# Kernel optimization log

Measured on AMD Instinct MI355X. Metric: run time of the kernel, lower is better.

## Reference

```python
import jax, jax.numpy as jnp
import numpy as np

N = 100000      # num_nodes
E = 1600000     # num_edges (avg degree 16)
IN = 128        # in_channels
HID = 8         # hidden_channels (per head)
HEADS = 8
OUT = 64        # out_channels
NEG_SLOPE = 0.2


def setup_inputs() -> dict:
    key = jax.random.key(0)
    ks = jax.random.split(key, 11)
    s = 0.05
    return {
        "x": jax.random.normal(ks[0], (N, IN), jnp.float32),
        "edge_index": jax.random.randint(ks[1], (2, E), 0, N, dtype=jnp.int32),
        "W1": jax.random.normal(ks[2], (IN, HEADS * HID), jnp.float32) * s,
        "a_src1": jax.random.normal(ks[3], (HEADS, HID), jnp.float32) * s,
        "a_dst1": jax.random.normal(ks[4], (HEADS, HID), jnp.float32) * s,
        "b1": jnp.zeros((HEADS * HID,), jnp.float32),
        "W2": jax.random.normal(ks[5], (HEADS * HID, OUT), jnp.float32) * s,
        "a_src2": jax.random.normal(ks[6], (1, OUT), jnp.float32) * s,
        "a_dst2": jax.random.normal(ks[7], (1, OUT), jnp.float32) * s,
        "b2": jnp.zeros((OUT,), jnp.float32),
    }


def gat_conv(x, src, dst, W, a_src, a_dst, bias, heads, out_ch):
    """PyG GATConv (concat=True, dropout=0, self-loops already in src/dst)."""
    n = x.shape[0]
    h = (x @ W).reshape(n, heads, out_ch)               # [N, H, C]
    al_src = jnp.einsum('nhc,hc->nh', h, a_src)          # [N, H]
    al_dst = jnp.einsum('nhc,hc->nh', h, a_dst)          # [N, H]
    e = jax.nn.leaky_relu(al_src[src] + al_dst[dst], NEG_SLOPE)  # [E, H]
    # segment softmax over destination nodes (numerically stable)
    e_max = jax.ops.segment_max(e, dst, num_segments=n)  # [N, H]
    ex = jnp.exp(e - e_max[dst])
    denom = jax.ops.segment_sum(ex, dst, num_segments=n)
    alpha = ex / (denom[dst] + 1e-16)                    # [E, H]
    msg = h[src] * alpha[:, :, None]                     # [E, H, C]
    out = jax.ops.segment_sum(msg, dst, num_segments=n)  # [N, H, C]
    return out.reshape(n, heads * out_ch) + bias


def reference(x, edge_index, W1, a_src1, a_dst1, b1, W2, a_src2, a_dst2, b2):
    n = x.shape[0]
    loops = jnp.arange(n, dtype=edge_index.dtype)
    src = jnp.concatenate([edge_index[0], loops])        # add self-loops (PyG default)
    dst = jnp.concatenate([edge_index[1], loops])
    h = gat_conv(x, src, dst, W1, a_src1, a_dst1, b1, HEADS, HID)
    h = jax.nn.elu(h)
    out = gat_conv(h, src, dst, W2, a_src2, a_dst2, b2, 1, OUT)
    return out
```

## Files before the change

### kernel.cpp

```cpp
#include <hip/hip_runtime.h>
#include <hip/hip_bf16.h>

#define IN_CH   128
#define HEADS   8
#define HID     8
#define MID_CH  64
#define OUT_CH  64
#define CAP     64
#define NRANGE  8

typedef unsigned short u16;
__device__ __forceinline__ u16 f2bu(float f) {
    union { float f; unsigned int i; } v; v.f = f;
    unsigned int lsb = (v.i >> 16) & 1u;
    return (u16)((v.i + 0x7fffu + lsb) >> 16);
}
__device__ __forceinline__ float2 up2(unsigned int u) {
    union { unsigned int i; float f; } a, b;
    a.i = u << 16; b.i = u & 0xffff0000u;
    return make_float2(a.f, b.f);
}
__device__ __forceinline__ float lrelu(float e) { return (e > 0.f) ? e : 0.2f * e; }

__global__ void k0_init(int* __restrict__ deg, int N) {
    int n = blockIdx.x * blockDim.x + threadIdx.x;
    if (n < N) deg[n] = 0;
}

__global__ __launch_bounds__(256) void k1_fill(
    const int* __restrict__ src, const int* __restrict__ dst,
    int* __restrict__ deg, int* __restrict__ adj, int E, int N) {
    int range = blockIdx.x & (NRANGE - 1);
    int chunk = blockIdx.x >> 3;
    int lo = (int)(((long long)N * range) >> 3);
    int hi = (int)(((long long)N * (range + 1)) >> 3);
    int t = chunk * 256 + threadIdx.x;
    int base = t * 4;
    if (base + 3 < E) {
        int4 d4 = *(const int4*)(dst + base);
        int4 s4 = *(const int4*)(src + base);
        if (d4.x >= lo && d4.x < hi) { int p = atomicAdd(&deg[d4.x], 1); if (p < CAP) adj[d4.x * CAP + p] = s4.x; }
        if (d4.y >= lo && d4.y < hi) { int p = atomicAdd(&deg[d4.y], 1); if (p < CAP) adj[d4.y * CAP + p] = s4.y; }
        if (d4.z >= lo && d4.z < hi) { int p = atomicAdd(&deg[d4.z], 1); if (p < CAP) adj[d4.z * CAP + p] = s4.z; }
        if (d4.w >= lo && d4.w < hi) { int p = atomicAdd(&deg[d4.w], 1); if (p < CAP) adj[d4.w * CAP + p] = s4.w; }
    } else {
        for (int j = 0; j < 4; j++) {
            int e = base + j;
            if (e < E) {
                int d = dst[e];
                if (d >= lo && d < hi) {
                    int p = atomicAdd(&deg[d], 1);
                    if (p < CAP) adj[d * CAP + p] = src[e];
                }
            }
        }
    }
}

__global__ __launch_bounds__(256) void k2_gemm1(
    const float* __restrict__ x, const float* __restrict__ W1,
    const float* __restrict__ a_src, const float* __restrict__ a_dst,
    u16* __restrict__ h1b, float* __restrict__ als, float* __restrict__ ald, int N)
{
    __shared__ float Wl[IN_CH * MID_CH];
    __shared__ float xl[16 * IN_CH];
    int tid = threadIdx.x;
    {
        const float4* W4 = (const float4*)W1;
        float4* Wl4 = (float4*)Wl;
        for (int i = tid; i < IN_CH * MID_CH / 4; i += 256) Wl4[i] = W4[i];
    }
    int base = blockIdx.x * 16;
    {
        float4* xl4 = (float4*)xl;
        const float4* x4 = (const float4*)x;
        for (int i = tid; i < 16 * IN_CH / 4; i += 256) {
            int r = i >> 5;
            int n = base + r;
            xl4[i] = (n < N) ? x4[(size_t)n * (IN_CH / 4) + (i & 31)]
                             : make_float4(0.f, 0.f, 0.f, 0.f);
        }
    }
    __syncthreads();

    int wave = tid >> 6, lane = tid & 63;
    int r0 = wave * 4;
    float acc[4] = {0.f, 0.f, 0.f, 0.f};
    const float* x0 = &xl[(r0 + 0) * IN_CH];
    const float* x1 = &xl[(r0 + 1) * IN_CH];
    const float* x2 = &xl[(r0 + 2) * IN_CH];
    const float* x3 = &xl[(r0 + 3) * IN_CH];
    #pragma unroll 8
    for (int k = 0; k < IN_CH; k++) {
        float w = Wl[k * MID_CH + lane];
        acc[0] += x0[k] * w;
        acc[1] += x1[k] * w;
        acc[2] += x2[k] * w;
        acc[3] += x3[k] * w;
    }
    float asv = a_src[lane];
    float adv = a_dst[lane];
    #pragma unroll
    for (int g = 0; g < 4; g++) {
        int n = base + r0 + g;
        if (n >= N) continue;
        h1b[(size_t)n * MID_CH + lane] = f2bu(acc[g]);
        float vs = acc[g] * asv;
        float vd = acc[g] * adv;
        vs += __shfl_xor(vs, 1); vs += __shfl_xor(vs, 2); vs += __shfl_xor(vs, 4);
        vd += __shfl_xor(vd, 1); vd += __shfl_xor(vd, 2); vd += __shfl_xor(vd, 4);
        if ((lane & 7) == 0) {
            als[n * HEADS + (lane >> 3)] = vs;
            ald[n * HEADS + (lane >> 3)] = vd;
        }
    }
}

__global__ __launch_bounds__(256) void k3_agg1(
    const int* __restrict__ deg, const int* __restrict__ adj,
    const u16* __restrict__ h1b, const float* __restrict__ als,
    const float* __restrict__ ald, const float* __restrict__ b1,
    float* __restrict__ h2, int N)
{
    __shared__ int adjl[4][CAP];
    int wave = threadIdx.x >> 6, lane = threadIdx.x & 63;
    int n = blockIdx.x * 4 + wave;
    bool valid = (n < N);
    int nc = valid ? n : (N - 1);

    int g = lane >> 3;
    int c8 = lane & 7;
    int dg = deg[nc]; if (dg > CAP) dg = CAP;
    if (lane < dg) adjl[wave][lane] = adj[(size_t)nc * CAP + lane];
    float aldv = ald[nc * HEADS + c8];
    __syncthreads();

    const uint4* h1v = (const uint4*)h1b;
    float acc[8] = {0,0,0,0,0,0,0,0};
    float denom = 0.f;
    for (int i = g; i < dg; i += 8) {
        int s = adjl[wave][i];
        float ex = __expf(lrelu(als[s * HEADS + c8] + aldv));
        uint4 q = h1v[(size_t)s * 8 + c8];
        float2 p0 = up2(q.x), p1 = up2(q.y), p2 = up2(q.z), p3 = up2(q.w);
        denom += ex;
        acc[0] += ex * p0.x; acc[1] += ex * p0.y;
        acc[2] += ex * p1.x; acc[3] += ex * p1.y;
        acc[4] += ex * p2.x; acc[5] += ex * p2.y;
        acc[6] += ex * p3.x; acc[7] += ex * p3.y;
    }
    if (g == 0) {
        float ex = __expf(lrelu(als[nc * HEADS + c8] + aldv));
        uint4 q = h1v[(size_t)nc * 8 + c8];
        float2 p0 = up2(q.x), p1 = up2(q.y), p2 = up2(q.z), p3 = up2(q.w);
        denom += ex;
        acc[0] += ex * p0.x; acc[1] += ex * p0.y;
        acc[2] += ex * p1.x; acc[3] += ex * p1.y;
        acc[4] += ex * p2.x; acc[5] += ex * p2.y;
        acc[6] += ex * p3.x; acc[7] += ex * p3.y;
    }
    denom += __shfl_xor(denom, 8); denom += __shfl_xor(denom, 16); denom += __shfl_xor(denom, 32);
    #pragma unroll
    for (int j = 0; j < 8; j++) {
        acc[j] += __shfl_xor(acc[j], 8);
        acc[j] += __shfl_xor(acc[j], 16);
        acc[j] += __shfl_xor(acc[j], 32);
    }
    float inv = 1.f / (denom + 1e-16f);

    if (g == 0 && valid) {
        const float4* b4 = (const float4*)b1;
        float4 bl = b4[c8 * 2], bh = b4[c8 * 2 + 1];
        float4 o0, o1;
        o0.x = acc[0] * inv + bl.x; o0.y = acc[1] * inv + bl.y;
        o0.z = acc[2] * inv + bl.z; o0.w = acc[3] * inv + bl.w;
        o1.x = acc[4] * inv + bh.x; o1.y = acc[5] * inv + bh.y;
        o1.z = acc[6] * inv + bh.z; o1.w = acc[7] * inv + bh.w;
        o0.x = (o0.x > 0.f) ? o0.x : (__expf(o0.x) - 1.f);
        o0.y = (o0.y > 0.f) ? o0.y : (__expf(o0.y) - 1.f);
        o0.z = (o0.z > 0.f) ? o0.z : (__expf(o0.z) - 1.f);
        o0.w = (o0.w > 0.f) ? o0.w : (__expf(o0.w) - 1.f);
        o1.x = (o1.x > 0.f) ? o1.x : (__expf(o1.x) - 1.f);
        o1.y = (o1.y > 0.f) ? o1.y : (__expf(o1.y) - 1.f);
        o1.z = (o1.z > 0.f) ? o1.z : (__expf(o1.z) - 1.f);
        o1.w = (o1.w > 0.f) ? o1.w : (__expf(o1.w) - 1.f);
        float4* h2v = (float4*)h2;
        h2v[(size_t)n * 16 + c8 * 2]     = o0;
        h2v[(size_t)n * 16 + c8 * 2 + 1] = o1;
    }
}

__global__ __launch_bounds__(256) void k4_gemm2(
    const float* __restrict__ h2, const float* __restrict__ W2,
    const float* __restrict__ a_src, const float* __restrict__ a_dst,
    u16* __restrict__ t2b, float* __restrict__ als, float* __restrict__ ald, int N)
{
    __shared__ float Wl[MID_CH * OUT_CH];
    __shared__ float xl[16 * MID_CH];
    int tid = threadIdx.x;
    {
        const float4* W4 = (const float4*)W2;
        float4* Wl4 = (float4*)Wl;
        for (int i = tid; i < MID_CH * OUT_CH / 4; i += 256) Wl4[i] = W4[i];
    }
    int base = blockIdx.x * 16;
    {
        float4* xl4 = (float4*)xl;
        const float4* x4 = (const float4*)h2;
        for (int i = tid; i < 16 * MID_CH / 4; i += 256) {
            int r = i >> 4;
            int n = base + r;
            xl4[i] = (n < N) ? x4[(size_t)n * (MID_CH / 4) + (i & 15)]
                             : make_float4(0.f, 0.f, 0.f, 0.f);
        }
    }
    __syncthreads();

    int wave = tid >> 6, lane = tid & 63;
    int r0 = wave * 4;
    float acc[4] = {0.f, 0.f, 0.f, 0.f};
    const float* x0 = &xl[(r0 + 0) * MID_CH];
    const float* x1 = &xl[(r0 + 1) * MID_CH];
    const float* x2 = &xl[(r0 + 2) * MID_CH];
    const float* x3 = &xl[(r0 + 3) * MID_CH];
    #pragma unroll 8
    for (int k = 0; k < MID_CH; k++) {
        float w = Wl[k * OUT_CH + lane];
        acc[0] += x0[k] * w;
        acc[1] += x1[k] * w;
        acc[2] += x2[k] * w;
        acc[3] += x3[k] * w;
    }
    float asv = a_src[lane];
    float adv = a_dst[lane];
    #pragma unroll
    for (int g = 0; g < 4; g++) {
        int n = base + r0 + g;
        if (n >= N) continue;
        t2b[(size_t)n * OUT_CH + lane] = f2bu(acc[g]);
        float vs = acc[g] * asv;
        float vd = acc[g] * adv;
        #pragma unroll
        for (int off = 1; off < 64; off <<= 1) {
            vs += __shfl_xor(vs, off);
            vd += __shfl_xor(vd, off);
        }
        if (lane == 0) { als[n] = vs; ald[n] = vd; }
    }
}

__global__ __launch_bounds__(256) void k5_agg2(
    const int* __restrict__ deg, const int* __restrict__ adj,
    const u16* __restrict__ t2b, const float* __restrict__ als,
    const float* __restrict__ ald, const float* __restrict__ b2,
    float* __restrict__ out, int N)
{
    __shared__ int adjl[4][CAP];
    int wave = threadIdx.x >> 6, lane = threadIdx.x & 63;
    int n = blockIdx.x * 4 + wave;
    bool valid = (n < N);
    int nc = valid ? n : (N - 1);

    int g = lane >> 3;
    int c8 = lane & 7;
    int dg = deg[nc]; if (dg > CAP) dg = CAP;
    if (lane < dg) adjl[wave][lane] = adj[(size_t)nc * CAP + lane];
    float aldv = ald[nc];
    __syncthreads();

    const uint4* t2v = (const uint4*)t2b;
    float acc[8] = {0,0,0,0,0,0,0,0};
    float denom = 0.f;
    for (int i = g; i < dg; i += 8) {
        int s = adjl[wave][i];
        float ex = __expf(lrelu(als[s] + aldv));
        uint4 q = t2v[(size_t)s * 8 + c8];
        float2 p0 = up2(q.x), p1 = up2(q.y), p2 = up2(q.z), p3 = up2(q.w);
        denom += ex;
        acc[0] += ex * p0.x; acc[1] += ex * p0.y;
        acc[2] += ex * p1.x; acc[3] += ex * p1.y;
        acc[4] += ex * p2.x; acc[5] += ex * p2.y;
        acc[6] += ex * p3.x; acc[7] += ex * p3.y;
    }
    if (g == 0) {
        float ex = __expf(lrelu(als[nc] + aldv));
        uint4 q = t2v[(size_t)nc * 8 + c8];
        float2 p0 = up2(q.x), p1 = up2(q.y), p2 = up2(q.z), p3 = up2(q.w);
        denom += ex;
        acc[0] += ex * p0.x; acc[1] += ex * p0.y;
        acc[2] += ex * p1.x; acc[3] += ex * p1.y;
        acc[4] += ex * p2.x; acc[5] += ex * p2.y;
        acc[6] += ex * p3.x; acc[7] += ex * p3.y;
    }
    denom += __shfl_xor(denom, 8); denom += __shfl_xor(denom, 16); denom += __shfl_xor(denom, 32);
    #pragma unroll
    for (int j = 0; j < 8; j++) {
        acc[j] += __shfl_xor(acc[j], 8);
        acc[j] += __shfl_xor(acc[j], 16);
        acc[j] += __shfl_xor(acc[j], 32);
    }
    float inv = 1.f / (denom + 1e-16f);

    if (g == 0 && valid) {
        const float4* b4 = (const float4*)b2;
        float4 bl = b4[c8 * 2], bh = b4[c8 * 2 + 1];
        float4 o0, o1;
        o0.x = acc[0] * inv + bl.x; o0.y = acc[1] * inv + bl.y;
        o0.z = acc[2] * inv + bl.z; o0.w = acc[3] * inv + bl.w;
        o1.x = acc[4] * inv + bh.x; o1.y = acc[5] * inv + bh.y;
        o1.z = acc[6] * inv + bh.z; o1.w = acc[7] * inv + bh.w;
        float4* ov = (float4*)out;
        ov[(size_t)n * 16 + c8 * 2]     = o0;
        ov[(size_t)n * 16 + c8 * 2 + 1] = o1;
    }
}

extern "C" void kernel_launch(void* const* d_in, const int* in_sizes, int n_in,
                              void* d_out, int out_size, void* d_ws, size_t ws_size,
                              hipStream_t stream) {
    const float* x   = (const float*)d_in[0];
    const int*   ei  = (const int*)d_in[1];
    const float* W1  = (const float*)d_in[2];
    const float* as1 = (const float*)d_in[3];
    const float* ad1 = (const float*)d_in[4];
    const float* b1  = (const float*)d_in[5];
    const float* W2  = (const float*)d_in[6];
    const float* as2 = (const float*)d_in[7];
    const float* ad2 = (const float*)d_in[8];
    const float* b2  = (const float*)d_in[9];
    float* out = (float*)d_out;

    int N = in_sizes[0] / IN_CH;
    int E = in_sizes[1] / 2;
    const int* srcp = ei;
    const int* dstp = ei + E;

    char* w = (char*)d_ws;
    size_t off = 0;
    auto alloc = [&](size_t bytes) {
        void* p = w + off;
        off += (bytes + 255) & ~(size_t)255;
        return p;
    };
    int*   deg  = (int*)  alloc((size_t)N * 4);
    int*   adj  = (int*)  alloc((size_t)N * CAP * 4);
    u16*   h1b  = (u16*)  alloc((size_t)N * MID_CH * 2);
    float* als1 = (float*)alloc((size_t)N * HEADS * 4);
    float* ald1 = (float*)alloc((size_t)N * HEADS * 4);
    float* h2   = (float*)alloc((size_t)N * MID_CH * 4);
    u16*   t2b  = (u16*)  alloc((size_t)N * OUT_CH * 2);
    float* als2 = (float*)alloc((size_t)N * 4);
    float* ald2 = (float*)alloc((size_t)N * 4);
    (void)ws_size; (void)n_in; (void)out_size;

    k0_init<<<(N + 255) / 256, 256, 0, stream>>>(deg, N);
    int chunks = (E + 1023) / 1024;
    k1_fill<<<chunks * NRANGE, 256, 0, stream>>>(srcp, dstp, deg, adj, E, N);
    k2_gemm1<<<(N + 15) / 16, 256, 0, stream>>>(x, W1, as1, ad1, h1b, als1, ald1, N);
    k3_agg1<<<(N + 3) / 4, 256, 0, stream>>>(deg, adj, h1b, als1, ald1, b1, h2, N);
    k4_gemm2<<<(N + 15) / 16, 256, 0, stream>>>(h2, W2, as2, ad2, t2b, als2, ald2, N);
    k5_agg2<<<(N + 3) / 4, 256, 0, stream>>>(deg, adj, t2b, als2, ald2, b2, out, N);
}
```

Baseline: 373.3 us.

## Read GEMM rows via scalar loads, skip unneeded src loads, memset degree

Removes the shared-memory staging of x and h2 rows in both GEMM kernels. Each wave now reads its four rows through wave-uniform (readfirstlane) pointers, which should become scalar loads, and the k-loop unroll goes from 8 to 16 with explicit FMAs. The fill kernel loads the src int4 only when at least one destination falls in the block's range, which cuts redundant src reads across the range-partitioned passes. The custom degree-zeroing kernel is replaced by hipMemsetAsync; the tradeoff is that scalar-load latency and cache behaviour for the GEMM rows are not guaranteed to beat shared-memory staging.

```diff
diff --git a/kernel.cpp b/kernel.cpp
--- a/kernel.cpp
+++ b/kernel.cpp
@@ -21,11 +21,6 @@
     return make_float2(a.f, b.f);
 }
 __device__ __forceinline__ float lrelu(float e) { return (e > 0.f) ? e : 0.2f * e; }
-
-__global__ void k0_init(int* __restrict__ deg, int N) {
-    int n = blockIdx.x * blockDim.x + threadIdx.x;
-    if (n < N) deg[n] = 0;
-}
 
 __global__ __launch_bounds__(256) void k1_fill(
     const int* __restrict__ src, const int* __restrict__ dst,
@@ -38,11 +33,17 @@
     int base = t * 4;
     if (base + 3 < E) {
         int4 d4 = *(const int4*)(dst + base);
-        int4 s4 = *(const int4*)(src + base);
-        if (d4.x >= lo && d4.x < hi) { int p = atomicAdd(&deg[d4.x], 1); if (p < CAP) adj[d4.x * CAP + p] = s4.x; }
-        if (d4.y >= lo && d4.y < hi) { int p = atomicAdd(&deg[d4.y], 1); if (p < CAP) adj[d4.y * CAP + p] = s4.y; }
-        if (d4.z >= lo && d4.z < hi) { int p = atomicAdd(&deg[d4.z], 1); if (p < CAP) adj[d4.z * CAP + p] = s4.z; }
-        if (d4.w >= lo && d4.w < hi) { int p = atomicAdd(&deg[d4.w], 1); if (p < CAP) adj[d4.w * CAP + p] = s4.w; }
+        bool ix = (d4.x >= lo && d4.x < hi);
+        bool iy = (d4.y >= lo && d4.y < hi);
+        bool iz = (d4.z >= lo && d4.z < hi);
+        bool iw = (d4.w >= lo && d4.w < hi);
+        if (ix | iy | iz | iw) {
+            int4 s4 = *(const int4*)(src + base);
+            if (ix) { int p = atomicAdd(&deg[d4.x], 1); if (p < CAP) adj[d4.x * CAP + p] = s4.x; }
+            if (iy) { int p = atomicAdd(&deg[d4.y], 1); if (p < CAP) adj[d4.y * CAP + p] = s4.y; }
+            if (iz) { int p = atomicAdd(&deg[d4.z], 1); if (p < CAP) adj[d4.z * CAP + p] = s4.z; }
+            if (iw) { int p = atomicAdd(&deg[d4.w], 1); if (p < CAP) adj[d4.w * CAP + p] = s4.w; }
+        }
     } else {
         for (int j = 0; j < 4; j++) {
             int e = base + j;
@@ -63,46 +64,41 @@
     u16* __restrict__ h1b, float* __restrict__ als, float* __restrict__ ald, int N)
 {
     __shared__ float Wl[IN_CH * MID_CH];
-    __shared__ float xl[16 * IN_CH];
     int tid = threadIdx.x;
     {
         const float4* W4 = (const float4*)W1;
         float4* Wl4 = (float4*)Wl;
         for (int i = tid; i < IN_CH * MID_CH / 4; i += 256) Wl4[i] = W4[i];
     }
+    __syncthreads();
+
+    int wave = tid >> 6, lane = tid & 63;
     int base = blockIdx.x * 16;
-    {
-        float4* xl4 = (float4*)xl;
-        const float4* x4 = (const float4*)x;
-        for (int i = tid; i < 16 * IN_CH / 4; i += 256) {
-            int r = i >> 5;
-            int n = base + r;
-            xl4[i] = (n < N) ? x4[(size_t)n * (IN_CH / 4) + (i & 31)]
-                             : make_float4(0.f, 0.f, 0.f, 0.f);
-        }
-    }
-    __syncthreads();
-
-    int wave = tid >> 6, lane = tid & 63;
     int r0 = wave * 4;
+    int n0 = base + r0;
+    int c0 = (n0 + 0 < N) ? (n0 + 0) : (N - 1);
+    int c1 = (n0 + 1 < N) ? (n0 + 1) : (N - 1);
+    int c2 = (n0 + 2 < N) ? (n0 + 2) : (N - 1);
+    int c3 = (n0 + 3 < N) ? (n0 + 3) : (N - 1);
+    const float* xr0 = x + (size_t)__builtin_amdgcn_readfirstlane(c0) * IN_CH;
+    const float* xr1 = x + (size_t)__builtin_amdgcn_readfirstlane(c1) * IN_CH;
+    const float* xr2 = x + (size_t)__builtin_amdgcn_readfirstlane(c2) * IN_CH;
+    const float* xr3 = x + (size_t)__builtin_amdgcn_readfirstlane(c3) * IN_CH;
+
     float acc[4] = {0.f, 0.f, 0.f, 0.f};
-    const float* x0 = &xl[(r0 + 0) * IN_CH];
-    const float* x1 = &xl[(r0 + 1) * IN_CH];
-    const float* x2 = &xl[(r0 + 2) * IN_CH];
-    const float* x3 = &xl[(r0 + 3) * IN_CH];
-    #pragma unroll 8
+    #pragma unroll 16
     for (int k = 0; k < IN_CH; k++) {
         float w = Wl[k * MID_CH + lane];
-        acc[0] += x0[k] * w;
-        acc[1] += x1[k] * w;
-        acc[2] += x2[k] * w;
-        acc[3] += x3[k] * w;
+        acc[0] = fmaf(xr0[k], w, acc[0]);
+        acc[1] = fmaf(xr1[k], w, acc[1]);
+        acc[2] = fmaf(xr2[k], w, acc[2]);
+        acc[3] = fmaf(xr3[k], w, acc[3]);
     }
     float asv = a_src[lane];
     float adv = a_dst[lane];
     #pragma unroll
     for (int g = 0; g < 4; g++) {
-        int n = base + r0 + g;
+        int n = n0 + g;
         if (n >= N) continue;
         h1b[(size_t)n * MID_CH + lane] = f2bu(acc[g]);
         float vs = acc[g] * asv;
@@ -196,46 +192,41 @@
     u16* __restrict__ t2b, float* __restrict__ als, float* __restrict__ ald, int N)
 {
     __shared__ float Wl[MID_CH * OUT_CH];
-    __shared__ float xl[16 * MID_CH];
     int tid = threadIdx.x;
     {
         const float4* W4 = (const float4*)W2;
         float4* Wl4 = (float4*)Wl;
         for (int i = tid; i < MID_CH * OUT_CH / 4; i += 256) Wl4[i] = W4[i];
     }
+    __syncthreads();
+
+    int wave = tid >> 6, lane = tid & 63;
     int base = blockIdx.x * 16;
-    {
-        float4* xl4 = (float4*)xl;
-        const float4* x4 = (const float4*)h2;
-        for (int i = tid; i < 16 * MID_CH / 4; i += 256) {
-            int r = i >> 4;
-            int n = base + r;
-            xl4[i] = (n < N) ? x4[(size_t)n * (MID_CH / 4) + (i & 15)]
-                             : make_float4(0.f, 0.f, 0.f, 0.f);
-        }
-    }
-    __syncthreads();
-
-    int wave = tid >> 6, lane = tid & 63;
     int r0 = wave * 4;
+    int n0 = base + r0;
+    int c0 = (n0 + 0 < N) ? (n0 + 0) : (N - 1);
+    int c1 = (n0 + 1 < N) ? (n0 + 1) : (N - 1);
+    int c2 = (n0 + 2 < N) ? (n0 + 2) : (N - 1);
+    int c3 = (n0 + 3 < N) ? (n0 + 3) : (N - 1);
+    const float* xr0 = h2 + (size_t)__builtin_amdgcn_readfirstlane(c0) * MID_CH;
+    const float* xr1 = h2 + (size_t)__builtin_amdgcn_readfirstlane(c1) * MID_CH;
+    const float* xr2 = h2 + (size_t)__builtin_amdgcn_readfirstlane(c2) * MID_CH;
+    const float* xr3 = h2 + (size_t)__builtin_amdgcn_readfirstlane(c3) * MID_CH;
+
     float acc[4] = {0.f, 0.f, 0.f, 0.f};
-    const float* x0 = &xl[(r0 + 0) * MID_CH];
-    const float* x1 = &xl[(r0 + 1) * MID_CH];
-    const float* x2 = &xl[(r0 + 2) * MID_CH];
-    const float* x3 = &xl[(r0 + 3) * MID_CH];
-    #pragma unroll 8
+    #pragma unroll 16
     for (int k = 0; k < MID_CH; k++) {
         float w = Wl[k * OUT_CH + lane];
-        acc[0] += x0[k] * w;
-        acc[1] += x1[k] * w;
-        acc[2] += x2[k] * w;
-        acc[3] += x3[k] * w;
+        acc[0] = fmaf(xr0[k], w, acc[0]);
+        acc[1] = fmaf(xr1[k], w, acc[1]);
+        acc[2] = fmaf(xr2[k], w, acc[2]);
+        acc[3] = fmaf(xr3[k], w, acc[3]);
     }
     float asv = a_src[lane];
     float adv = a_dst[lane];
     #pragma unroll
     for (int g = 0; g < 4; g++) {
-        int n = base + r0 + g;
+        int n = n0 + g;
         if (n >= N) continue;
         t2b[(size_t)n * OUT_CH + lane] = f2bu(acc[g]);
         float vs = acc[g] * asv;
@@ -353,7 +344,7 @@
     float* ald2 = (float*)alloc((size_t)N * 4);
     (void)ws_size; (void)n_in; (void)out_size;
 
-    k0_init<<<(N + 255) / 256, 256, 0, stream>>>(deg, N);
+    hipMemsetAsync(deg, 0, (size_t)N * 4, stream);
     int chunks = (E + 1023) / 1024;
     k1_fill<<<chunks * NRANGE, 256, 0, stream>>>(srcp, dstp, deg, adj, E, N);
     k2_gemm1<<<(N + 15) / 16, 256, 0, stream>>>(x, W1, as1, ad1, h1b, als1, ald1, N);
```

After: 387.6 us. 3.8% more time.

## Vectorize GEMM LDS reads, skip src loads for out-of-range edges, memset degrees

Applied to the files above, without the earlier changes.

The two small GEMM kernels now read x rows from shared memory as float4 and use explicit fmaf over four k-steps, which cuts the number of LDS instructions. The edge-fill kernel loads the src int4 only when at least one of the four destinations falls in the block's node range, avoiding redundant src reads across the 8 range passes. The degree-init kernel is replaced by hipMemsetAsync, and unroll pragmas are added to the staging loops. The changes are small and local; the GEMMs are likely a minor share of total time next to the aggregation kernels.

```diff
diff --git a/kernel.cpp b/kernel.cpp
--- a/kernel.cpp
+++ b/kernel.cpp
@@ -21,11 +21,6 @@
     return make_float2(a.f, b.f);
 }
 __device__ __forceinline__ float lrelu(float e) { return (e > 0.f) ? e : 0.2f * e; }
-
-__global__ void k0_init(int* __restrict__ deg, int N) {
-    int n = blockIdx.x * blockDim.x + threadIdx.x;
-    if (n < N) deg[n] = 0;
-}
 
 __global__ __launch_bounds__(256) void k1_fill(
     const int* __restrict__ src, const int* __restrict__ dst,
@@ -38,11 +33,17 @@
     int base = t * 4;
     if (base + 3 < E) {
         int4 d4 = *(const int4*)(dst + base);
-        int4 s4 = *(const int4*)(src + base);
-        if (d4.x >= lo && d4.x < hi) { int p = atomicAdd(&deg[d4.x], 1); if (p < CAP) adj[d4.x * CAP + p] = s4.x; }
-        if (d4.y >= lo && d4.y < hi) { int p = atomicAdd(&deg[d4.y], 1); if (p < CAP) adj[d4.y * CAP + p] = s4.y; }
-        if (d4.z >= lo && d4.z < hi) { int p = atomicAdd(&deg[d4.z], 1); if (p < CAP) adj[d4.z * CAP + p] = s4.z; }
-        if (d4.w >= lo && d4.w < hi) { int p = atomicAdd(&deg[d4.w], 1); if (p < CAP) adj[d4.w * CAP + p] = s4.w; }
+        bool ix = (d4.x >= lo && d4.x < hi);
+        bool iy = (d4.y >= lo && d4.y < hi);
+        bool iz = (d4.z >= lo && d4.z < hi);
+        bool iw = (d4.w >= lo && d4.w < hi);
+        if (ix | iy | iz | iw) {
+            int4 s4 = *(const int4*)(src + base);
+            if (ix) { int p = atomicAdd(&deg[d4.x], 1); if (p < CAP) adj[d4.x * CAP + p] = s4.x; }
+            if (iy) { int p = atomicAdd(&deg[d4.y], 1); if (p < CAP) adj[d4.y * CAP + p] = s4.y; }
+            if (iz) { int p = atomicAdd(&deg[d4.z], 1); if (p < CAP) adj[d4.z * CAP + p] = s4.z; }
+            if (iw) { int p = atomicAdd(&deg[d4.w], 1); if (p < CAP) adj[d4.w * CAP + p] = s4.w; }
+        }
     } else {
         for (int j = 0; j < 4; j++) {
             int e = base + j;
@@ -68,12 +69,14 @@
     {
         const float4* W4 = (const float4*)W1;
         float4* Wl4 = (float4*)Wl;
+        #pragma unroll
         for (int i = tid; i < IN_CH * MID_CH / 4; i += 256) Wl4[i] = W4[i];
     }
     int base = blockIdx.x * 16;
     {
         float4* xl4 = (float4*)xl;
         const float4* x4 = (const float4*)x;
+        #pragma unroll
         for (int i = tid; i < 16 * IN_CH / 4; i += 256) {
             int r = i >> 5;
             int n = base + r;
@@ -85,28 +88,40 @@
 
     int wave = tid >> 6, lane = tid & 63;
     int r0 = wave * 4;
-    float acc[4] = {0.f, 0.f, 0.f, 0.f};
-    const float* x0 = &xl[(r0 + 0) * IN_CH];
-    const float* x1 = &xl[(r0 + 1) * IN_CH];
-    const float* x2 = &xl[(r0 + 2) * IN_CH];
-    const float* x3 = &xl[(r0 + 3) * IN_CH];
+    const float* xr0 = &xl[(r0 + 0) * IN_CH];
+    const float* xr1 = &xl[(r0 + 1) * IN_CH];
+    const float* xr2 = &xl[(r0 + 2) * IN_CH];
+    const float* xr3 = &xl[(r0 + 3) * IN_CH];
+    float acc0 = 0.f, acc1 = 0.f, acc2 = 0.f, acc3 = 0.f;
     #pragma unroll 8
-    for (int k = 0; k < IN_CH; k++) {
-        float w = Wl[k * MID_CH + lane];
-        acc[0] += x0[k] * w;
-        acc[1] += x1[k] * w;
-        acc[2] += x2[k] * w;
-        acc[3] += x3[k] * w;
-    }
+    for (int kc = 0; kc < IN_CH; kc += 4) {
+        float4 xa = *(const float4*)(xr0 + kc);
+        float4 xb = *(const float4*)(xr1 + kc);
+        float4 xc = *(const float4*)(xr2 + kc);
+        float4 xd = *(const float4*)(xr3 + kc);
+        float w0 = Wl[(kc + 0) * MID_CH + lane];
+        float w1 = Wl[(kc + 1) * MID_CH + lane];
+        float w2 = Wl[(kc + 2) * MID_CH + lane];
+        float w3 = Wl[(kc + 3) * MID_CH + lane];
+        acc0 = fmaf(xa.x, w0, acc0); acc0 = fmaf(xa.y, w1, acc0);
+        acc0 = fmaf(xa.z, w2, acc0); acc0 = fmaf(xa.w, w3, acc0);
+        acc1 = fmaf(xb.x, w0, acc1); acc1 = fmaf(xb.y, w1, acc1);
+        acc1 = fmaf(xb.z, w2, acc1); acc1 = fmaf(xb.w, w3, acc1);
+        acc2 = fmaf(xc.x, w0, acc2); acc2 = fmaf(xc.y, w1, acc2);
+        acc2 = fmaf(xc.z, w2, acc2); acc2 = fmaf(xc.w, w3, acc2);
+        acc3 = fmaf(xd.x, w0, acc3); acc3 = fmaf(xd.y, w1, acc3);
+        acc3 = fmaf(xd.z, w2, acc3); acc3 = fmaf(xd.w, w3, acc3);
+    }
+    float accs[4] = {acc0, acc1, acc2, acc3};
     float asv = a_src[lane];
     float adv = a_dst[lane];
     #pragma unroll
     for (int g = 0; g < 4; g++) {
         int n = base + r0 + g;
         if (n >= N) continue;
-        h1b[(size_t)n * MID_CH + lane] = f2bu(acc[g]);
-        float vs = acc[g] * asv;
-        float vd = acc[g] * adv;
+        h1b[(size_t)n * MID_CH + lane] = f2bu(accs[g]);
+        float vs = accs[g] * asv;
+        float vd = accs[g] * adv;
         vs += __shfl_xor(vs, 1); vs += __shfl_xor(vs, 2); vs += __shfl_xor(vs, 4);
         vd += __shfl_xor(vd, 1); vd += __shfl_xor(vd, 2); vd += __shfl_xor(vd, 4);
         if ((lane & 7) == 0) {
@@ -201,12 +216,14 @@
     {
         const float4* W4 = (const float4*)W2;
         float4* Wl4 = (float4*)Wl;
+        #pragma unroll
         for (int i = tid; i < MID_CH * OUT_CH / 4; i += 256) Wl4[i] = W4[i];
     }
     int base = blockIdx.x * 16;
     {
         float4* xl4 = (float4*)xl;
         const float4* x4 = (const float4*)h2;
+        #pragma unroll
         for (int i = tid; i < 16 * MID_CH / 4; i += 256) {
             int r = i >> 4;
             int n = base + r;
@@ -218,28 +235,40 @@
 
     int wave = tid >> 6, lane = tid & 63;
     int r0 = wave * 4;
-    float acc[4] = {0.f, 0.f, 0.f, 0.f};
-    const float* x0 = &xl[(r0 + 0) * MID_CH];
-    const float* x1 = &xl[(r0 + 1) * MID_CH];
-    const float* x2 = &xl[(r0 + 2) * MID_CH];
-    const float* x3 = &xl[(r0 + 3) * MID_CH];
+    const float* xr0 = &xl[(r0 + 0) * MID_CH];
+    const float* xr1 = &xl[(r0 + 1) * MID_CH];
+    const float* xr2 = &xl[(r0 + 2) * MID_CH];
+    const float* xr3 = &xl[(r0 + 3) * MID_CH];
+    float acc0 = 0.f, acc1 = 0.f, acc2 = 0.f, acc3 = 0.f;
     #pragma unroll 8
-    for (int k = 0; k < MID_CH; k++) {
-        float w = Wl[k * OUT_CH + lane];
-        acc[0] += x0[k] * w;
-        acc[1] += x1[k] * w;
-        acc[2] += x2[k] * w;
-        acc[3] += x3[k] * w;
-    }
+    for (int kc = 0; kc < MID_CH; kc += 4) {
+        float4 xa = *(const float4*)(xr0 + kc);
+        float4 xb = *(const float4*)(xr1 + kc);
+        float4 xc = *(const float4*)(xr2 + kc);
+        float4 xd = *(const float4*)(xr3 + kc);
+        float w0 = Wl[(kc + 0) * OUT_CH + lane];
+        float w1 = Wl[(kc + 1) * OUT_CH + lane];
+        float w2 = Wl[(kc + 2) * OUT_CH + lane];
+        float w3 = Wl[(kc + 3) * OUT_CH + lane];
+        acc0 = fmaf(xa.x, w0, acc0); acc0 = fmaf(xa.y, w1, acc0);
+        acc0 = fmaf(xa.z, w2, acc0); acc0 = fmaf(xa.w, w3, acc0);
+        acc1 = fmaf(xb.x, w0, acc1); acc1 = fmaf(xb.y, w1, acc1);
+        acc1 = fmaf(xb.z, w2, acc1); acc1 = fmaf(xb.w, w3, acc1);
+        acc2 = fmaf(xc.x, w0, acc2); acc2 = fmaf(xc.y, w1, acc2);
+        acc2 = fmaf(xc.z, w2, acc2); acc2 = fmaf(xc.w, w3, acc2);
+        acc3 = fmaf(xd.x, w0, acc3); acc3 = fmaf(xd.y, w1, acc3);
+        acc3 = fmaf(xd.z, w2, acc3); acc3 = fmaf(xd.w, w3, acc3);
+    }
+    float accs[4] = {acc0, acc1, acc2, acc3};
     float asv = a_src[lane];
     float adv = a_dst[lane];
     #pragma unroll
     for (int g = 0; g < 4; g++) {
         int n = base + r0 + g;
         if (n >= N) continue;
-        t2b[(size_t)n * OUT_CH + lane] = f2bu(acc[g]);
-        float vs = acc[g] * asv;
-        float vd = acc[g] * adv;
+        t2b[(size_t)n * OUT_CH + lane] = f2bu(accs[g]);
+        float vs = accs[g] * asv;
+        float vd = accs[g] * adv;
         #pragma unroll
         for (int off = 1; off < 64; off <<= 1) {
             vs += __shfl_xor(vs, off);
@@ -353,7 +382,7 @@
     float* ald2 = (float*)alloc((size_t)N * 4);
     (void)ws_size; (void)n_in; (void)out_size;
 
-    k0_init<<<(N + 255) / 256, 256, 0, stream>>>(deg, N);
+    hipMemsetAsync(deg, 0, (size_t)N * 4, stream);
     int chunks = (E + 1023) / 1024;
     k1_fill<<<chunks * NRANGE, 256, 0, stream>>>(srcp, dstp, deg, adj, E, N);
     k2_gemm1<<<(N + 15) / 16, 256, 0, stream>>>(x, W1, as1, ad1, h1b, als1, ald1, N);
```

After: 370.3 us. Within noise of the previous version (-0.8%).
